# Performance work log

Hardware: AMD Instinct MI355X
Metric: run time of the kernel (lower is better)

The kernel has to match this reference:

```python
import jax, jax.numpy as jnp
import numpy as np

NEG_SLOPE = 0.2  # PyG GATConv default negative_slope


def _gat_layer(x, src, dst, W, a_src, a_dst, b, heads, ch, concat, num_nodes):
    # x: [Nt, Fin]; W: [Fin, heads*ch]; a_src/a_dst: [heads, ch]
    xw = (x @ W).reshape(num_nodes, heads, ch)            # [Nt, H, C]
    alpha_s = jnp.sum(xw * a_src, axis=-1)                # [Nt, H]
    alpha_d = jnp.sum(xw * a_dst, axis=-1)                # [Nt, H]
    e = jax.nn.leaky_relu(alpha_s[src] + alpha_d[dst], NEG_SLOPE)  # [E, H]
    # segment softmax over destination nodes (every node has a self-loop)
    m = jax.lax.stop_gradient(jax.ops.segment_max(e, dst, num_segments=num_nodes))
    ex = jnp.exp(e - m[dst])
    denom = jax.ops.segment_sum(ex, dst, num_segments=num_nodes)
    alpha = ex / (denom[dst] + 1e-16)                     # [E, H]
    out = jax.ops.segment_sum(alpha[:, :, None] * xw[src], dst, num_segments=num_nodes)  # [Nt, H, C]
    out = out.reshape(num_nodes, heads * ch) if concat else out.mean(axis=1)
    return out + b


def setup_inputs() -> dict:
    key = jax.random.key(0)
    ks = jax.random.split(key, 12)
    B, N, IN, HID, H, OUT, E = 2, 10000, 256, 256, 2, 256, 160000
    x = jax.random.normal(ks[0], (B, N, IN), dtype=jnp.float32)
    edge_index = jax.random.randint(ks[1], (2, E), 0, N, dtype=jnp.int32)
    s_in = 1.0 / np.sqrt(IN)
    s_h = 1.0 / np.sqrt(HID)
    s_hh = 1.0 / np.sqrt(HID * H)
    W1 = jax.random.normal(ks[2], (IN, H * HID), dtype=jnp.float32) * s_in
    att_src1 = jax.random.normal(ks[3], (H, HID), dtype=jnp.float32) * s_h
    att_dst1 = jax.random.normal(ks[4], (H, HID), dtype=jnp.float32) * s_h
    b1 = jax.random.normal(ks[5], (H * HID,), dtype=jnp.float32) * 0.01
    W2 = jax.random.normal(ks[6], (H * HID, OUT), dtype=jnp.float32) * s_hh
    att_src2 = jax.random.normal(ks[7], (1, OUT), dtype=jnp.float32) * s_h
    att_dst2 = jax.random.normal(ks[8], (1, OUT), dtype=jnp.float32) * s_h
    b2 = jax.random.normal(ks[9], (OUT,), dtype=jnp.float32) * 0.01
    return {"x": x, "edge_index": edge_index, "W1": W1, "att_src1": att_src1,
            "att_dst1": att_dst1, "b1": b1, "W2": W2, "att_src2": att_src2,
            "att_dst2": att_dst2, "b2": b2}


def reference(x, edge_index, W1, att_src1, att_dst1, b1, W2, att_src2, att_dst2, b2):
    B, N, C = x.shape
    H, HID = att_src1.shape
    OUT = W2.shape[1]
    Nt = B * N
    xf = x.reshape(Nt, C)
    # batch edge index with per-graph node offsets (shared edges across batch)
    offs = (jnp.arange(B, dtype=edge_index.dtype) * N)       # [B]
    ei = (edge_index[:, None, :] + offs[None, :, None]).reshape(2, -1)  # [2, B*E]
    # add self loops (PyG GATConv default)
    loops = jnp.arange(Nt, dtype=edge_index.dtype)
    src = jnp.concatenate([ei[0], loops])
    dst = jnp.concatenate([ei[1], loops])
    h = _gat_layer(xf, src, dst, W1, att_src1, att_dst1, b1, H, HID, True, Nt)
    h = jax.nn.gelu(h, approximate=False)  # torch F.gelu default = exact erf
    out = _gat_layer(h, src, dst, W2, att_src2, att_dst2, b2, 1, OUT, False, Nt)
    return out.reshape(B, N, OUT)
```

## Files before the change

### kernel.cpp

```cpp
#include <hip/hip_runtime.h>
#include <math.h>

constexpr int B_   = 2;
constexpr int N_   = 10000;
constexpr int IN_  = 256;
constexpr int HID_ = 256;
constexpr int H1_  = 2;
constexpr int OUT_ = 256;
constexpr int E_   = 160000;
constexpr int NT_  = B_ * N_;
constexpr float SLOPE = 0.2f;
constexpr int DMAX = 128;

typedef unsigned short u16;
typedef __attribute__((ext_vector_type(8))) short short8;
typedef __attribute__((ext_vector_type(4))) float f32x4;

__device__ __forceinline__ u16 f2bf(float f) {
    unsigned int u = __float_as_uint(f);
    u += 0x7fffu + ((u >> 16) & 1u);
    return (u16)(u >> 16);
}
__device__ __forceinline__ void bf8(uint4 r, float4& lo, float4& hi) {
    lo = make_float4(__uint_as_float((r.x & 0xffffu) << 16),
                     __uint_as_float(r.x & 0xffff0000u),
                     __uint_as_float((r.y & 0xffffu) << 16),
                     __uint_as_float(r.y & 0xffff0000u));
    hi = make_float4(__uint_as_float((r.z & 0xffffu) << 16),
                     __uint_as_float(r.z & 0xffff0000u),
                     __uint_as_float((r.w & 0xffffu) << 16),
                     __uint_as_float(r.w & 0xffff0000u));
}
__device__ __forceinline__ void fma4(float4& a, float s, float4 v) {
    a.x = fmaf(s, v.x, a.x); a.y = fmaf(s, v.y, a.y);
    a.z = fmaf(s, v.z, a.z); a.w = fmaf(s, v.w, a.w);
}
__device__ __forceinline__ float lrelu(float e) { return (e < 0.f) ? SLOPE * e : e; }

__device__ __forceinline__ void g2l16(const void* g, void* l) {
    __builtin_amdgcn_global_load_lds(
        (const __attribute__((address_space(1))) unsigned int*)g,
        (__attribute__((address_space(3))) unsigned int*)l, 16, 0, 0);
}

__global__ __launch_bounds__(256) void k_wprep(
    const float* __restrict__ W1,
    const float* __restrict__ aS1, const float* __restrict__ aD1,
    const float* __restrict__ W2,
    const float* __restrict__ aS2, const float* __restrict__ aD2,
    float* __restrict__ w1s, float* __restrict__ w1d,
    float* __restrict__ w2s, float* __restrict__ w2d,
    u16* __restrict__ W1t, u16* __restrict__ W2t,
    uint4* __restrict__ zbase) {
    __shared__ float tld[32][33];
    const int blk = blockIdx.x;
    if (blk < 16) {
        for (int i = blk * 256 + threadIdx.x; i < 12500; i += 16 * 256)
            zbase[i] = make_uint4(0, 0, 0, 0);
    } else if (blk < 528) {
        int wv = (blk - 16) * 4 + (threadIdx.x >> 6);
        int lane = threadIdx.x & 63;
        int c = lane * 4;
        float4 wr, av;
        if (wv < 1024) {
            int h = (wv >> 8) & 1;
            int k = wv & 255;
            const float* a = (wv < 512) ? aS1 : aD1;
            wr = *(const float4*)(W1 + (size_t)k * 512 + h * 256 + c);
            av = *(const float4*)(a + h * 256 + c);
        } else {
            int k = (wv - 1024) & 511;
            const float* a = (wv < 1536) ? aS2 : aD2;
            wr = *(const float4*)(W2 + (size_t)k * 256 + c);
            av = *(const float4*)(a + c);
        }
        float s = wr.x * av.x + wr.y * av.y + wr.z * av.z + wr.w * av.w;
        #pragma unroll
        for (int off = 32; off; off >>= 1) s += __shfl_down(s, off);
        if (lane == 0) {
            if (wv < 512)       w1s[wv] = s;
            else if (wv < 1024) w1d[wv - 512] = s;
            else if (wv < 1536) w2s[wv - 1024] = s;
            else                w2d[wv - 1536] = s;
        }
    } else {
        const int b = blk - 528;
        const int z = b >> 7;
        const int bb = b & 127;
        const float* S = z ? W2 : W1;
        u16* D = z ? W2t : W1t;
        const int R = z ? 512 : 256;
        const int C = z ? 256 : 512;
        const int xt = C >> 5;
        const int bx = bb % xt, by = bb / xt;
        const int tx = threadIdx.x & 31, ty = threadIdx.x >> 5;
        int xx = bx * 32 + tx;
        int y0 = by * 32 + ty;
        #pragma unroll
        for (int i = 0; i < 32; i += 8)
            tld[ty + i][tx] = S[(size_t)(y0 + i) * C + xx];
        __syncthreads();
        int xo = by * 32 + tx;
        int yo = bx * 32 + ty;
        #pragma unroll
        for (int i = 0; i < 32; i += 8)
            D[(size_t)(yo + i) * R + xo] = f2bf(tld[tx][ty + i]);
    }
}

__global__ __launch_bounds__(256) void k_pre(
    const float* __restrict__ x, u16* __restrict__ Xb,
    const float* __restrict__ w1s, const float* __restrict__ w1d,
    float* __restrict__ as1, float* __restrict__ ad1,
    const int* __restrict__ ei, int* __restrict__ cnt, int* __restrict__ bucket) {
    const int NB = NT_ / 4;
    if ((int)blockIdx.x < NB) {
        const int w = threadIdx.x >> 6, lane = threadIdx.x & 63;
        const int nt = blockIdx.x * 4 + w;
        const int c = lane * 4;
        float4 v = *(const float4*)(x + (size_t)nt * 256 + c);
        ((uint2*)(Xb + (size_t)nt * 256))[lane] =
            make_uint2((unsigned)f2bf(v.x) | ((unsigned)f2bf(v.y) << 16),
                       (unsigned)f2bf(v.z) | ((unsigned)f2bf(v.w) << 16));
        float4 s0v = *(const float4*)(w1s + c);
        float4 s1v = *(const float4*)(w1s + 256 + c);
        float4 d0v = *(const float4*)(w1d + c);
        float4 d1v = *(const float4*)(w1d + 256 + c);
        float s0 = v.x*s0v.x + v.y*s0v.y + v.z*s0v.z + v.w*s0v.w;
        float s1 = v.x*s1v.x + v.y*s1v.y + v.z*s1v.z + v.w*s1v.w;
        float d0 = v.x*d0v.x + v.y*d0v.y + v.z*d0v.z + v.w*d0v.w;
        float d1 = v.x*d1v.x + v.y*d1v.y + v.z*d1v.z + v.w*d1v.w;
        #pragma unroll
        for (int off = 32; off; off >>= 1) {
            s0 += __shfl_down(s0, off); s1 += __shfl_down(s1, off);
            d0 += __shfl_down(d0, off); d1 += __shfl_down(d1, off);
        }
        if (lane == 0) {
            as1[nt * 2] = s0; as1[nt * 2 + 1] = s1;
            ad1[nt * 2] = d0; ad1[nt * 2 + 1] = d1;
        }
    } else {
        int e = (blockIdx.x - NB) * 256 + threadIdx.x;
        if (e < E_) {
            int s = ei[e], d = ei[E_ + e];
            int p = atomicAdd(&cnt[d], 1);
            if (p < DMAX - 1) bucket[d * DMAX + p] = s;
        }
    }
}

__global__ __launch_bounds__(256) void k_agg1x(
    const u16* __restrict__ Xb,
    const float* __restrict__ as_, const float* __restrict__ ad_,
    const int* __restrict__ cnt, const int* __restrict__ bucket,
    u16* __restrict__ Y) {
    __shared__ int   stl[4][DMAX];
    __shared__ float exw[4][2 * DMAX];
    const int w    = threadIdx.x >> 6;
    const int lane = threadIdx.x & 63;
    const int half = lane >> 5;
    const int l32  = lane & 31;
    const int nt   = blockIdx.x * 4 + w;
    if (nt >= NT_) return;
    const int nl   = nt % N_;
    const int boff = nt - nl;
    const int r0   = nl * DMAX;
    int deg = cnt[nl]; deg = (deg < DMAX - 1) ? deg : (DMAX - 1);
    const float adv0 = ad_[nt * 2], adv1 = ad_[nt * 2 + 1];
    const float adv = half ? adv1 : adv0;

    for (int i = lane; i <= deg; i += 64)
        stl[w][i] = (i < deg) ? (bucket[r0 + i] + boff) : nt;

    float den = 0.f;
    for (int i = l32; i <= deg; i += 32) {
        int st = stl[w][i];
        float ex = __expf(lrelu(as_[st * 2 + half] + adv));
        exw[w][2 * i + half] = ex;
        den += ex;
    }
    #pragma unroll
    for (int off = 16; off; off >>= 1) den += __shfl_xor(den, off);
    const float inv = 1.f / (den + 1e-16f);
    const float invO = __shfl_xor(inv, 32);

    const int slot = half;
    const int nin = deg + 1;
    const u16* fb = Xb + l32 * 8;
    float4 A0l = {0,0,0,0}, A0h = {0,0,0,0}, A1l = {0,0,0,0}, A1h = {0,0,0,0};
    float4 B0l = {0,0,0,0}, B0h = {0,0,0,0}, B1l = {0,0,0,0}, B1h = {0,0,0,0};
    int j = 0;
    for (; j + 8 <= nin; j += 8) {
        int sA = stl[w][j + slot],     sB = stl[w][j + 2 + slot];
        int sC = stl[w][j + 4 + slot], sD = stl[w][j + 6 + slot];
        float2 wA = *(const float2*)&exw[w][2 * (j + slot)];
        float2 wB = *(const float2*)&exw[w][2 * (j + 2 + slot)];
        float2 wC = *(const float2*)&exw[w][2 * (j + 4 + slot)];
        float2 wD = *(const float2*)&exw[w][2 * (j + 6 + slot)];
        uint4 vA = *(const uint4*)(fb + (size_t)sA * 256);
        uint4 vB = *(const uint4*)(fb + (size_t)sB * 256);
        uint4 vC = *(const uint4*)(fb + (size_t)sC * 256);
        uint4 vD = *(const uint4*)(fb + (size_t)sD * 256);
        float4 lo, hi;
        bf8(vA, lo, hi); fma4(A0l, wA.x, lo); fma4(A0h, wA.x, hi);
                         fma4(A1l, wA.y, lo); fma4(A1h, wA.y, hi);
        bf8(vB, lo, hi); fma4(B0l, wB.x, lo); fma4(B0h, wB.x, hi);
                         fma4(B1l, wB.y, lo); fma4(B1h, wB.y, hi);
        bf8(vC, lo, hi); fma4(A0l, wC.x, lo); fma4(A0h, wC.x, hi);
                         fma4(A1l, wC.y, lo); fma4(A1h, wC.y, hi);
        bf8(vD, lo, hi); fma4(B0l, wD.x, lo); fma4(B0h, wD.x, hi);
                         fma4(B1l, wD.y, lo); fma4(B1h, wD.y, hi);
    }
    for (int jj = j + slot; jj < nin; jj += 2) {
        int s0 = stl[w][jj];
        float2 w01 = *(const float2*)&exw[w][2 * jj];
        uint4 v0 = *(const uint4*)(fb + (size_t)s0 * 256);
        float4 lo, hi;
        bf8(v0, lo, hi); fma4(A0l, w01.x, lo); fma4(A0h, w01.x, hi);
                         fma4(A1l, w01.y, lo); fma4(A1h, w01.y, hi);
    }
    A0l.x += B0l.x; A0l.y += B0l.y; A0l.z += B0l.z; A0l.w += B0l.w;
    A0h.x += B0h.x; A0h.y += B0h.y; A0h.z += B0h.z; A0h.w += B0h.w;
    A1l.x += B1l.x; A1l.y += B1l.y; A1l.z += B1l.z; A1l.w += B1l.w;
    A1h.x += B1h.x; A1h.y += B1h.y; A1h.z += B1h.z; A1h.w += B1h.w;
    A0l.x += __shfl_xor(A0l.x, 32); A0l.y += __shfl_xor(A0l.y, 32);
    A0l.z += __shfl_xor(A0l.z, 32); A0l.w += __shfl_xor(A0l.w, 32);
    A0h.x += __shfl_xor(A0h.x, 32); A0h.y += __shfl_xor(A0h.y, 32);
    A0h.z += __shfl_xor(A0h.z, 32); A0h.w += __shfl_xor(A0h.w, 32);
    A1l.x += __shfl_xor(A1l.x, 32); A1l.y += __shfl_xor(A1l.y, 32);
    A1l.z += __shfl_xor(A1l.z, 32); A1l.w += __shfl_xor(A1l.w, 32);
    A1h.x += __shfl_xor(A1h.x, 32); A1h.y += __shfl_xor(A1h.y, 32);
    A1h.z += __shfl_xor(A1h.z, 32); A1h.w += __shfl_xor(A1h.w, 32);

    if (slot == 0) {
        float f0[8] = { A0l.x*inv,  A0l.y*inv,  A0l.z*inv,  A0l.w*inv,
                        A0h.x*inv,  A0h.y*inv,  A0h.z*inv,  A0h.w*inv };
        float f1[8] = { A1l.x*invO, A1l.y*invO, A1l.z*invO, A1l.w*invO,
                        A1h.x*invO, A1h.y*invO, A1h.z*invO, A1h.w*invO };
        size_t ob = (size_t)nt * 512 + l32 * 8;
        *(uint4*)(Y + ob) =
            make_uint4((unsigned)f2bf(f0[0]) | ((unsigned)f2bf(f0[1]) << 16),
                       (unsigned)f2bf(f0[2]) | ((unsigned)f2bf(f0[3]) << 16),
                       (unsigned)f2bf(f0[4]) | ((unsigned)f2bf(f0[5]) << 16),
                       (unsigned)f2bf(f0[6]) | ((unsigned)f2bf(f0[7]) << 16));
        *(uint4*)(Y + ob + 256) =
            make_uint4((unsigned)f2bf(f1[0]) | ((unsigned)f2bf(f1[1]) << 16),
                       (unsigned)f2bf(f1[2]) | ((unsigned)f2bf(f1[3]) << 16),
                       (unsigned)f2bf(f1[4]) | ((unsigned)f2bf(f1[5]) << 16),
                       (unsigned)f2bf(f1[6]) | ((unsigned)f2bf(f1[7]) << 16));
    }
}

__global__ __launch_bounds__(256, 3) void gemm_g(
    const u16* __restrict__ Yf, const u16* __restrict__ W1t,
    u16* __restrict__ Hb,
    const float* __restrict__ b1,
    const float* __restrict__ w2s, const float* __restrict__ w2d,
    float* __restrict__ as2, float* __restrict__ ad2, int M) {
    __shared__ u16 sA[64 * 256];
    __shared__ u16 sBd[2][64 * 64];
    const int tid = threadIdx.x, wave = tid >> 6, lane = tid & 63;
    const int bm = blockIdx.x, h = blockIdx.y;
    const int wm = wave & 1, wn = wave >> 1;
    const int l15 = lane & 15, quad = lane >> 4;

    {
        const int rl = lane >> 5;
        const int u  = lane & 31;
        #pragma unroll
        for (int i = 0; i < 8; i++) {
            int rloc = wave * 16 + i * 2 + rl;
            int rg = bm * 64 + rloc; rg = (rg < M) ? rg : (M - 1);
            int us = (u & ~7) | ((u & 7) ^ (rloc & 7));
            g2l16(Yf + (size_t)rg * 512 + h * 256 + us * 8,
                  &sA[(wave * 16 + i * 2) * 256]);
        }
    }

    const int brl = lane >> 3;
    const int bu  = lane & 7;
    auto stageB = [&](int bn, int kb, int b) {
        #pragma unroll
        for (int i = 0; i < 2; i++) {
            int R0 = wave * 16 + i * 8;
            int r = R0 + brl;
            int us = bu ^ (r & 7);
            g2l16(W1t + (size_t)(h * 256 + bn * 64 + r) * 256 + kb * 64 + us * 8,
                  &sBd[b][R0 * 64]);
        }
    };

    const int rA0 = wm * 32 + l15, rA1 = rA0 + 16;
    const int rB0 = wn * 32 + l15, rB1 = rB0 + 16;

    f32x4 acc[2][2];
    #pragma unroll
    for (int i = 0; i < 2; i++)
        #pragma unroll
        for (int j = 0; j < 2; j++)
            acc[i][j] = (f32x4){0.f, 0.f, 0.f, 0.f};

    stageB(0, 0, 0);
    __syncthreads();
    int buf = 0;
    for (int bn = 0; bn < 4; bn++) {
        #pragma unroll
        for (int kb = 0; kb < 4; kb++) {
            int nbn = (kb == 3) ? bn + 1 : bn;
            int nkb = (kb == 3) ? 0 : kb + 1;
            if (nbn < 4) stageB(nbn, nkb, buf ^ 1);
            #pragma unroll
            for (int ks = 0; ks < 2; ks++) {
                int ua = kb * 8 + ks * 4 + quad;
                short8 a0 = *(const short8*)(&sA[rA0 * 256 + ((ua & ~7) | ((ua & 7) ^ (rA0 & 7))) * 8]);
                short8 a1 = *(const short8*)(&sA[rA1 * 256 + ((ua & ~7) | ((ua & 7) ^ (rA1 & 7))) * 8]);
                int ub = ks * 4 + quad;
                short8 b0  = *(const short8*)(&sBd[buf][rB0 * 64 + (ub ^ (rB0 & 7)) * 8]);
                short8 b1v = *(const short8*)(&sBd[buf][rB1 * 64 + (ub ^ (rB1 & 7)) * 8]);
                acc[0][0] = __builtin_amdgcn_mfma_f32_16x16x32_bf16(a0, b0,  acc[0][0], 0, 0, 0);
                acc[0][1] = __builtin_amdgcn_mfma_f32_16x16x32_bf16(a0, b1v, acc[0][1], 0, 0, 0);
                acc[1][0] = __builtin_amdgcn_mfma_f32_16x16x32_bf16(a1, b0,  acc[1][0], 0, 0, 0);
                acc[1][1] = __builtin_amdgcn_mfma_f32_16x16x32_bf16(a1, b1v, acc[1][1], 0, 0, 0);
            }
            if (kb == 3) {
                const int colL = bn * 64 + wn * 32;
                float Bv[2], Sv[2], Dv[2];
                #pragma unroll
                for (int j = 0; j < 2; j++) {
                    int cg = h * 256 + colL + j * 16 + l15;
                    Bv[j] = b1[cg]; Sv[j] = w2s[cg]; Dv[j] = w2d[cg];
                }
                #pragma unroll
                for (int i = 0; i < 2; i++) {
                    #pragma unroll
                    for (int r = 0; r < 4; r++) {
                        int row = bm * 64 + wm * 32 + i * 16 + quad * 4 + r;
                        float o[2], ps = 0.f, pd = 0.f;
                        #pragma unroll
                        for (int j = 0; j < 2; j++) {
                            float v = acc[i][j][r] + Bv[j];
                            v = 0.5f * v * (1.f + erff(v * 0.70710678118654752f));
                            o[j] = v;
                            ps = fmaf(v, Sv[j], ps);
                            pd = fmaf(v, Dv[j], pd);
                        }
                        #pragma unroll
                        for (int off = 1; off < 16; off <<= 1) {
                            ps += __shfl_xor(ps, off);
                            pd += __shfl_xor(pd, off);
                        }
                        if (row < M) {
                            if (l15 == 0) { atomicAdd(&as2[row], ps); atomicAdd(&ad2[row], pd); }
                            #pragma unroll
                            for (int j = 0; j < 2; j++)
                                Hb[(size_t)row * 512 + h * 256 + colL + j * 16 + l15] = f2bf(o[j]);
                        }
                    }
                }
                #pragma unroll
                for (int i = 0; i < 2; i++)
                    #pragma unroll
                    for (int j = 0; j < 2; j++)
                        acc[i][j] = (f32x4){0.f, 0.f, 0.f, 0.f};
            }
            __syncthreads();
            buf ^= 1;
        }
    }
}

__global__ __launch_bounds__(256, 3) void gemm_p(
    const u16* __restrict__ A, const u16* __restrict__ Bt,
    u16* __restrict__ C16, int M) {
    __shared__ u16 sA[32 * 512];
    __shared__ u16 sBd[2][64 * 64];
    const int tid = threadIdx.x, wave = tid >> 6, lane = tid & 63;
    const int bm = blockIdx.x;
    const int wm = wave & 1, wn = wave >> 1;
    const int l15 = lane & 15, quad = lane >> 4;

    {
        const int u = lane;
        #pragma unroll
        for (int i = 0; i < 8; i++) {
            int rloc = wave * 8 + i;
            int rg = bm * 32 + rloc; rg = (rg < M) ? rg : (M - 1);
            int us = (u & ~7) | ((u & 7) ^ (rloc & 7));
            g2l16(A + (size_t)rg * 512 + us * 8, &sA[rloc * 512]);
        }
    }

    const int brl = lane >> 3;
    const int bu  = lane & 7;
    auto stageB = [&](int bn, int kb, int b) {
        #pragma unroll
        for (int i = 0; i < 2; i++) {
            int R0 = wave * 16 + i * 8;
            int r = R0 + brl;
            int us = bu ^ (r & 7);
            g2l16(Bt + (size_t)(bn * 64 + r) * 512 + kb * 64 + us * 8,
                  &sBd[b][R0 * 64]);
        }
    };

    const int rA0 = wm * 16 + l15;
    const int rB0 = wn * 32 + l15, rB1 = rB0 + 16;

    f32x4 acc[2];
    acc[0] = (f32x4){0.f, 0.f, 0.f, 0.f};
    acc[1] = (f32x4){0.f, 0.f, 0.f, 0.f};

    stageB(0, 0, 0);
    __syncthreads();
    int buf = 0;
    for (int bn = 0; bn < 4; bn++) {
        #pragma unroll
        for (int kb = 0; kb < 8; kb++) {
            int nbn = (kb == 7) ? bn + 1 : bn;
            int nkb = (kb == 7) ? 0 : kb + 1;
            if (nbn < 4) stageB(nbn, nkb, buf ^ 1);
            #pragma unroll
            for (int ks = 0; ks < 2; ks++) {
                int ua = kb * 8 + ks * 4 + quad;
                short8 a0 = *(const short8*)(&sA[rA0 * 512 + ((ua & ~7) | ((ua & 7) ^ (rA0 & 7))) * 8]);
                int ub = ks * 4 + quad;
                short8 b0  = *(const short8*)(&sBd[buf][rB0 * 64 + (ub ^ (rB0 & 7)) * 8]);
                short8 b1v = *(const short8*)(&sBd[buf][rB1 * 64 + (ub ^ (rB1 & 7)) * 8]);
                acc[0] = __builtin_amdgcn_mfma_f32_16x16x32_bf16(a0, b0,  acc[0], 0, 0, 0);
                acc[1] = __builtin_amdgcn_mfma_f32_16x16x32_bf16(a0, b1v, acc[1], 0, 0, 0);
            }
            if (kb == 7) {
                #pragma unroll
                for (int r = 0; r < 4; r++) {
                    int row = bm * 32 + wm * 16 + quad * 4 + r;
                    if (row < M) {
                        #pragma unroll
                        for (int j = 0; j < 2; j++) {
                            int col = bn * 64 + wn * 32 + j * 16 + l15;
                            C16[(size_t)row * 256 + col] = f2bf(acc[j][r]);
                        }
                    }
                }
                acc[0] = (f32x4){0.f, 0.f, 0.f, 0.f};
                acc[1] = (f32x4){0.f, 0.f, 0.f, 0.f};
            }
            __syncthreads();
            buf ^= 1;
        }
    }
}

__global__ __launch_bounds__(256) void k_agg_h1(
    const u16* __restrict__ feat,
    const float* __restrict__ as_, const float* __restrict__ ad_,
    const int* __restrict__ cnt, const int* __restrict__ bucket,
    const float* __restrict__ bias,
    float* __restrict__ out) {
    __shared__ int   stl[4][DMAX];
    __shared__ float exw[4][DMAX];
    const int w    = threadIdx.x >> 6;
    const int lane = threadIdx.x & 63;
    const int slot = lane >> 5;
    const int l32  = lane & 31;
    const int nt   = blockIdx.x * 4 + w;
    if (nt >= NT_) return;
    const int nl   = nt % N_;
    const int boff = nt - nl;
    const int r0   = nl * DMAX;
    int deg = cnt[nl]; deg = (deg < DMAX - 1) ? deg : (DMAX - 1);
    const float adv = ad_[nt];

    for (int i = lane; i <= deg; i += 64)
        stl[w][i] = (i < deg) ? (bucket[r0 + i] + boff) : nt;

    float den = 0.f;
    for (int i = lane; i <= deg; i += 64) {
        int st = stl[w][i];
        float ex = __expf(lrelu(as_[st] + adv));
        exw[w][i] = ex;
        den += ex;
    }
    #pragma unroll
    for (int off = 32; off; off >>= 1) den += __shfl_xor(den, off);
    const float inv = 1.f / (den + 1e-16f);

    const int nin = deg + 1;
    const u16* fb = feat + l32 * 8;
    float4 aA0 = {0,0,0,0}, aB0 = {0,0,0,0}, aA1 = {0,0,0,0}, aB1 = {0,0,0,0};
    int j = 0;
    for (; j + 8 <= nin; j += 8) {
        int sA = stl[w][j + slot],     sB = stl[w][j + 2 + slot];
        int sC = stl[w][j + 4 + slot], sD = stl[w][j + 6 + slot];
        float wA = exw[w][j + slot],     wB = exw[w][j + 2 + slot];
        float wC = exw[w][j + 4 + slot], wD = exw[w][j + 6 + slot];
        uint4 vA = *(const uint4*)(fb + (size_t)sA * 256);
        uint4 vB = *(const uint4*)(fb + (size_t)sB * 256);
        uint4 vC = *(const uint4*)(fb + (size_t)sC * 256);
        uint4 vD = *(const uint4*)(fb + (size_t)sD * 256);
        float4 lo, hi;
        bf8(vA, lo, hi); fma4(aA0, wA, lo); fma4(aB0, wA, hi);
        bf8(vB, lo, hi); fma4(aA1, wB, lo); fma4(aB1, wB, hi);
        bf8(vC, lo, hi); fma4(aA0, wC, lo); fma4(aB0, wC, hi);
        bf8(vD, lo, hi); fma4(aA1, wD, lo); fma4(aB1, wD, hi);
    }
    for (; j + 4 <= nin; j += 4) {
        int sA = stl[w][j + slot], sB = stl[w][j + 2 + slot];
        float wA = exw[w][j + slot], wB = exw[w][j + 2 + slot];
        uint4 vA = *(const uint4*)(fb + (size_t)sA * 256);
        uint4 vB = *(const uint4*)(fb + (size_t)sB * 256);
        float4 lo, hi;
        bf8(vA, lo, hi); fma4(aA0, wA, lo); fma4(aB0, wA, hi);
        bf8(vB, lo, hi); fma4(aA1, wB, lo); fma4(aB1, wB, hi);
    }
    for (int jj = j + slot; jj < nin; jj += 2) {
        int s0 = stl[w][jj];
        float w0 = exw[w][jj];
        uint4 v0 = *(const uint4*)(fb + (size_t)s0 * 256);
        float4 lo, hi;
        bf8(v0, lo, hi); fma4(aA0, w0, lo); fma4(aB0, w0, hi);
    }
    aA0.x += aA1.x; aA0.y += aA1.y; aA0.z += aA1.z; aA0.w += aA1.w;
    aB0.x += aB1.x; aB0.y += aB1.y; aB0.z += aB1.z; aB0.w += aB1.w;
    aA0.x += __shfl_xor(aA0.x, 32); aA0.y += __shfl_xor(aA0.y, 32);
    aA0.z += __shfl_xor(aA0.z, 32); aA0.w += __shfl_xor(aA0.w, 32);
    aB0.x += __shfl_xor(aB0.x, 32); aB0.y += __shfl_xor(aB0.y, 32);
    aB0.z += __shfl_xor(aB0.z, 32); aB0.w += __shfl_xor(aB0.w, 32);

    if (slot == 0) {
        int c = l32 * 8;
        float4 b0 = *(const float4*)(bias + c);
        float4 b1 = *(const float4*)(bias + c + 4);
        float* ob = out + (size_t)nt * 256 + c;
        *(float4*)(ob)     = make_float4(aA0.x * inv + b0.x, aA0.y * inv + b0.y,
                                         aA0.z * inv + b0.z, aA0.w * inv + b0.w);
        *(float4*)(ob + 4) = make_float4(aB0.x * inv + b1.x, aB0.y * inv + b1.y,
                                         aB0.z * inv + b1.z, aB0.w * inv + b1.w);
    }
}

extern "C" void kernel_launch(void* const* d_in, const int* in_sizes, int n_in,
                              void* d_out, int out_size, void* d_ws, size_t ws_size,
                              hipStream_t stream) {
    const float* x    = (const float*)d_in[0];
    const int*   ei   = (const int*)  d_in[1];
    const float* W1   = (const float*)d_in[2];
    const float* aS1  = (const float*)d_in[3];
    const float* aD1  = (const float*)d_in[4];
    const float* b1   = (const float*)d_in[5];
    const float* W2   = (const float*)d_in[6];
    const float* aS2  = (const float*)d_in[7];
    const float* aD2  = (const float*)d_in[8];
    const float* b2   = (const float*)d_in[9];
    float* out = (float*)d_out;

    u16* Xb   = (u16*)d_ws;
    u16* Y    = Xb + (size_t)NT_ * 256;
    u16* Hb   = Y  + (size_t)NT_ * 512;
    u16* hw16 = Hb + (size_t)NT_ * 512;
    float* as1 = (float*)(hw16 + (size_t)NT_ * 256);
    float* ad1 = as1 + NT_ * H1_;
    float* as2 = ad1 + NT_ * H1_;
    float* ad2 = as2 + NT_;
    int* cnt   = (int*)(ad2 + NT_);
    int* bucket= cnt + N_;
    u16* W1t   = (u16*)(bucket + N_ * DMAX);
    u16* W2t   = W1t + 512 * 256;
    float* w1s = (float*)(W2t + 256 * 512);
    float* w1d = w1s + 512;
    float* w2s = w1d + 512;
    float* w2d = w2s + 512;

    k_wprep<<<784, 256, 0, stream>>>(W1, aS1, aD1, W2, aS2, aD2,
                                     w1s, w1d, w2s, w2d, W1t, W2t, (uint4*)as2);

    k_pre<<<NT_ / 4 + (E_ + 255) / 256, 256, 0, stream>>>(
        x, Xb, w1s, w1d, as1, ad1, ei, cnt, bucket);

    k_agg1x<<<(NT_ + 3) / 4, 256, 0, stream>>>(Xb, as1, ad1, cnt, bucket, Y);
    gemm_g<<<dim3((NT_ + 63) / 64, 2), 256, 0, stream>>>(
        Y, W1t, Hb, b1, w2s, w2d, as2, ad2, NT_);

    gemm_p<<<dim3((NT_ + 31) / 32), 256, 0, stream>>>(Hb, W2t, hw16, NT_);
    k_agg_h1<<<(NT_ + 3) / 4, 256, 0, stream>>>(hw16, as2, ad2, cnt, bucket, b2, out);
}
```

Measured before the change: 192.1 us.

## Split aggregation kernels into four column slices with 8-row-parallel gather per wave

Both edge-aggregation kernels now launch four blocks per group of nodes, and each block handles one 64-column slice of the 256-wide features. Within a wave, 8 lanes cover a slice and 8 neighbour rows are gathered in parallel, then reduced with xor-shuffles. The aim is more parallelism and memory-level concurrency per node, since average degree is about 9, and less per-thread serial looping. In exchange, the softmax weights and neighbour list are recomputed four times per node, the unrolled multi-accumulator loops are dropped, and the cross-lane reduction is deeper.

Measured after the change: 240.3 us. +25.1%, slower.

```diff
diff --git a/kernel.cpp b/kernel.cpp
--- a/kernel.cpp
+++ b/kernel.cpp
@@ -149,25 +149,26 @@
     }
 }
 
-__global__ __launch_bounds__(256) void k_agg1x(
+__global__ __launch_bounds__(256) void k_agg1s(
     const u16* __restrict__ Xb,
     const float* __restrict__ as_, const float* __restrict__ ad_,
     const int* __restrict__ cnt, const int* __restrict__ bucket,
     u16* __restrict__ Y) {
     __shared__ int   stl[4][DMAX];
     __shared__ float exw[4][2 * DMAX];
-    const int w    = threadIdx.x >> 6;
-    const int lane = threadIdx.x & 63;
-    const int half = lane >> 5;
-    const int l32  = lane & 31;
-    const int nt   = blockIdx.x * 4 + w;
+    const int slice = blockIdx.x & 3;
+    const int grp   = blockIdx.x >> 2;
+    const int w     = threadIdx.x >> 6;
+    const int lane  = threadIdx.x & 63;
+    const int half  = lane >> 5;
+    const int l32   = lane & 31;
+    const int nt    = grp * 4 + w;
     if (nt >= NT_) return;
     const int nl   = nt % N_;
     const int boff = nt - nl;
     const int r0   = nl * DMAX;
     int deg = cnt[nl]; deg = (deg < DMAX - 1) ? deg : (DMAX - 1);
-    const float adv0 = ad_[nt * 2], adv1 = ad_[nt * 2 + 1];
-    const float adv = half ? adv1 : adv0;
+    const float adv = half ? ad_[nt * 2 + 1] : ad_[nt * 2];
 
     for (int i = lane; i <= deg; i += 64)
         stl[w][i] = (i < deg) ? (bucket[r0 + i] + boff) : nt;
@@ -181,63 +182,45 @@
     }
     #pragma unroll
     for (int off = 16; off; off >>= 1) den += __shfl_xor(den, off);
-    const float inv = 1.f / (den + 1e-16f);
-    const float invO = __shfl_xor(inv, 32);
-
-    const int slot = half;
-    const int nin = deg + 1;
-    const u16* fb = Xb + l32 * 8;
-    float4 A0l = {0,0,0,0}, A0h = {0,0,0,0}, A1l = {0,0,0,0}, A1h = {0,0,0,0};
-    float4 B0l = {0,0,0,0}, B0h = {0,0,0,0}, B1l = {0,0,0,0}, B1h = {0,0,0,0};
-    int j = 0;
-    for (; j + 8 <= nin; j += 8) {
-        int sA = stl[w][j + slot],     sB = stl[w][j + 2 + slot];
-        int sC = stl[w][j + 4 + slot], sD = stl[w][j + 6 + slot];
-        float2 wA = *(const float2*)&exw[w][2 * (j + slot)];
-        float2 wB = *(const float2*)&exw[w][2 * (j + 2 + slot)];
-        float2 wC = *(const float2*)&exw[w][2 * (j + 4 + slot)];
-        float2 wD = *(const float2*)&exw[w][2 * (j + 6 + slot)];
-        uint4 vA = *(const uint4*)(fb + (size_t)sA * 256);
-        uint4 vB = *(const uint4*)(fb + (size_t)sB * 256);
-        uint4 vC = *(const uint4*)(fb + (size_t)sC * 256);
-        uint4 vD = *(const uint4*)(fb + (size_t)sD * 256);
-        float4 lo, hi;
-        bf8(vA, lo, hi); fma4(A0l, wA.x, lo); fma4(A0h, wA.x, hi);
-                         fma4(A1l, wA.y, lo); fma4(A1h, wA.y, hi);
-        bf8(vB, lo, hi); fma4(B0l, wB.x, lo); fma4(B0h, wB.x, hi);
-                         fma4(B1l, wB.y, lo); fma4(B1h, wB.y, hi);
-        bf8(vC, lo, hi); fma4(A0l, wC.x, lo); fma4(A0h, wC.x, hi);
-                         fma4(A1l, wC.y, lo); fma4(A1h, wC.y, hi);
-        bf8(vD, lo, hi); fma4(B0l, wD.x, lo); fma4(B0h, wD.x, hi);
-                         fma4(B1l, wD.y, lo); fma4(B1h, wD.y, hi);
-    }
-    for (int jj = j + slot; jj < nin; jj += 2) {
-        int s0 = stl[w][jj];
-        float2 w01 = *(const float2*)&exw[w][2 * jj];
-        uint4 v0 = *(const uint4*)(fb + (size_t)s0 * 256);
-        float4 lo, hi;
-        bf8(v0, lo, hi); fma4(A0l, w01.x, lo); fma4(A0h, w01.x, hi);
-                         fma4(A1l, w01.y, lo); fma4(A1h, w01.y, hi);
-    }
-    A0l.x += B0l.x; A0l.y += B0l.y; A0l.z += B0l.z; A0l.w += B0l.w;
-    A0h.x += B0h.x; A0h.y += B0h.y; A0h.z += B0h.z; A0h.w += B0h.w;
-    A1l.x += B1l.x; A1l.y += B1l.y; A1l.z += B1l.z; A1l.w += B1l.w;
-    A1h.x += B1h.x; A1h.y += B1h.y; A1h.z += B1h.z; A1h.w += B1h.w;
-    A0l.x += __shfl_xor(A0l.x, 32); A0l.y += __shfl_xor(A0l.y, 32);
-    A0l.z += __shfl_xor(A0l.z, 32); A0l.w += __shfl_xor(A0l.w, 32);
-    A0h.x += __shfl_xor(A0h.x, 32); A0h.y += __shfl_xor(A0h.y, 32);
-    A0h.z += __shfl_xor(A0h.z, 32); A0h.w += __shfl_xor(A0h.w, 32);
-    A1l.x += __shfl_xor(A1l.x, 32); A1l.y += __shfl_xor(A1l.y, 32);
-    A1l.z += __shfl_xor(A1l.z, 32); A1l.w += __shfl_xor(A1l.w, 32);
-    A1h.x += __shfl_xor(A1h.x, 32); A1h.y += __shfl_xor(A1h.y, 32);
-    A1h.z += __shfl_xor(A1h.z, 32); A1h.w += __shfl_xor(A1h.w, 32);
-
-    if (slot == 0) {
-        float f0[8] = { A0l.x*inv,  A0l.y*inv,  A0l.z*inv,  A0l.w*inv,
-                        A0h.x*inv,  A0h.y*inv,  A0h.z*inv,  A0h.w*inv };
-        float f1[8] = { A1l.x*invO, A1l.y*invO, A1l.z*invO, A1l.w*invO,
-                        A1h.x*invO, A1h.y*invO, A1h.z*invO, A1h.w*invO };
-        size_t ob = (size_t)nt * 512 + l32 * 8;
+    const float inv  = 1.f / (den + 1e-16f);
+    const float inv0 = __shfl(inv, 0);
+    const float inv1 = __shfl(inv, 32);
+
+    const int rs = lane >> 3;
+    const int u  = lane & 7;
+    const u16* fb = Xb + slice * 64 + u * 8;
+    float4 a0l = {0,0,0,0}, a0h = {0,0,0,0};
+    float4 a1l = {0,0,0,0}, a1h = {0,0,0,0};
+    for (int j = 0; j <= deg; j += 8) {
+        int i = j + rs;
+        if (i <= deg) {
+            int st = stl[w][i];
+            float2 wp = *(const float2*)&exw[w][2 * i];
+            uint4 v = *(const uint4*)(fb + (size_t)st * 256);
+            float4 lo, hi;
+            bf8(v, lo, hi);
+            fma4(a0l, wp.x, lo); fma4(a0h, wp.x, hi);
+            fma4(a1l, wp.y, lo); fma4(a1h, wp.y, hi);
+        }
+    }
+    #pragma unroll
+    for (int off = 8; off < 64; off <<= 1) {
+        a0l.x += __shfl_xor(a0l.x, off); a0l.y += __shfl_xor(a0l.y, off);
+        a0l.z += __shfl_xor(a0l.z, off); a0l.w += __shfl_xor(a0l.w, off);
+        a0h.x += __shfl_xor(a0h.x, off); a0h.y += __shfl_xor(a0h.y, off);
+        a0h.z += __shfl_xor(a0h.z, off); a0h.w += __shfl_xor(a0h.w, off);
+        a1l.x += __shfl_xor(a1l.x, off); a1l.y += __shfl_xor(a1l.y, off);
+        a1l.z += __shfl_xor(a1l.z, off); a1l.w += __shfl_xor(a1l.w, off);
+        a1h.x += __shfl_xor(a1h.x, off); a1h.y += __shfl_xor(a1h.y, off);
+        a1h.z += __shfl_xor(a1h.z, off); a1h.w += __shfl_xor(a1h.w, off);
+    }
+
+    if (rs == 0) {
+        float f0[8] = { a0l.x*inv0, a0l.y*inv0, a0l.z*inv0, a0l.w*inv0,
+                        a0h.x*inv0, a0h.y*inv0, a0h.z*inv0, a0h.w*inv0 };
+        float f1[8] = { a1l.x*inv1, a1l.y*inv1, a1l.z*inv1, a1l.w*inv1,
+                        a1h.x*inv1, a1h.y*inv1, a1h.z*inv1, a1h.w*inv1 };
+        size_t ob = (size_t)nt * 512 + slice * 64 + u * 8;
         *(uint4*)(Y + ob) =
             make_uint4((unsigned)f2bf(f0[0]) | ((unsigned)f2bf(f0[1]) << 16),
                        (unsigned)f2bf(f0[2]) | ((unsigned)f2bf(f0[3]) << 16),
@@ -450,7 +433,7 @@
     }
 }
 
-__global__ __launch_bounds__(256) void k_agg_h1(
+__global__ __launch_bounds__(256) void k_agg2s(
     const u16* __restrict__ feat,
     const float* __restrict__ as_, const float* __restrict__ ad_,
     const int* __restrict__ cnt, const int* __restrict__ bucket,
@@ -458,11 +441,11 @@
     float* __restrict__ out) {
     __shared__ int   stl[4][DMAX];
     __shared__ float exw[4][DMAX];
-    const int w    = threadIdx.x >> 6;
-    const int lane = threadIdx.x & 63;
-    const int slot = lane >> 5;
-    const int l32  = lane & 31;
-    const int nt   = blockIdx.x * 4 + w;
+    const int slice = blockIdx.x & 3;
+    const int grp   = blockIdx.x >> 2;
+    const int w     = threadIdx.x >> 6;
+    const int lane  = threadIdx.x & 63;
+    const int nt    = grp * 4 + w;
     if (nt >= NT_) return;
     const int nl   = nt % N_;
     const int boff = nt - nl;
@@ -484,57 +467,38 @@
     for (int off = 32; off; off >>= 1) den += __shfl_xor(den, off);
     const float inv = 1.f / (den + 1e-16f);
 
-    const int nin = deg + 1;
-    const u16* fb = feat + l32 * 8;
-    float4 aA0 = {0,0,0,0}, aB0 = {0,0,0,0}, aA1 = {0,0,0,0}, aB1 = {0,0,0,0};
-    int j = 0;
-    for (; j + 8 <= nin; j += 8) {
-        int sA = stl[w][j + slot],     sB = stl[w][j + 2 + slot];
-        int sC = stl[w][j + 4 + slot], sD = stl[w][j + 6 + slot];
-        float wA = exw[w][j + slot],     wB = exw[w][j + 2 + slot];
-        float wC = exw[w][j + 4 + slot], wD = exw[w][j + 6 + slot];
-        uint4 vA = *(const uint4*)(fb + (size_t)sA * 256);
-        uint4 vB = *(const uint4*)(fb + (size_t)sB * 256);
-        uint4 vC = *(const uint4*)(fb + (size_t)sC * 256);
-        uint4 vD = *(const uint4*)(fb + (size_t)sD * 256);
-        float4 lo, hi;
-        bf8(vA, lo, hi); fma4(aA0, wA, lo); fma4(aB0, wA, hi);
-        bf8(vB, lo, hi); fma4(aA1, wB, lo); fma4(aB1, wB, hi);
-        bf8(vC, lo, hi); fma4(aA0, wC, lo); fma4(aB0, wC, hi);
-        bf8(vD, lo, hi); fma4(aA1, wD, lo); fma4(aB1, wD, hi);
-    }
-    for (; j + 4 <= nin; j += 4) {
-        int sA = stl[w][j + slot], sB = stl[w][j + 2 + slot];
-        float wA = exw[w][j + slot], wB = exw[w][j + 2 + slot];
-        uint4 vA = *(const uint4*)(fb + (size_t)sA * 256);
-        uint4 vB = *(const uint4*)(fb + (size_t)sB * 256);
-        float4 lo, hi;
-        bf8(vA, lo, hi); fma4(aA0, wA, lo); fma4(aB0, wA, hi);
-        bf8(vB, lo, hi); fma4(aA1, wB, lo); fma4(aB1, wB, hi);
-    }
-    for (int jj = j + slot; jj < nin; jj += 2) {
-        int s0 = stl[w][jj];
-        float w0 = exw[w][jj];
-        uint4 v0 = *(const uint4*)(fb + (size_t)s0 * 256);
-        float4 lo, hi;
-        bf8(v0, lo, hi); fma4(aA0, w0, lo); fma4(aB0, w0, hi);
-    }
-    aA0.x += aA1.x; aA0.y += aA1.y; aA0.z += aA1.z; aA0.w += aA1.w;
-    aB0.x += aB1.x; aB0.y += aB1.y; aB0.z += aB1.z; aB0.w += aB1.w;
-    aA0.x += __shfl_xor(aA0.x, 32); aA0.y += __shfl_xor(aA0.y, 32);
-    aA0.z += __shfl_xor(aA0.z, 32); aA0.w += __shfl_xor(aA0.w, 32);
-    aB0.x += __shfl_xor(aB0.x, 32); aB0.y += __shfl_xor(aB0.y, 32);
-    aB0.z += __shfl_xor(aB0.z, 32); aB0.w += __shfl_xor(aB0.w, 32);
-
-    if (slot == 0) {
-        int c = l32 * 8;
+    const int rs = lane >> 3;
+    const int u  = lane & 7;
+    const u16* fb = feat + slice * 64 + u * 8;
+    float4 al = {0,0,0,0}, ah = {0,0,0,0};
+    for (int j = 0; j <= deg; j += 8) {
+        int i = j + rs;
+        if (i <= deg) {
+            int st = stl[w][i];
+            float w0 = exw[w][i];
+            uint4 v = *(const uint4*)(fb + (size_t)st * 256);
+            float4 lo, hi;
+            bf8(v, lo, hi);
+            fma4(al, w0, lo); fma4(ah, w0, hi);
+        }
+    }
+    #pragma unroll
+    for (int off = 8; off < 64; off <<= 1) {
+        al.x += __shfl_xor(al.x, off); al.y += __shfl_xor(al.y, off);
+        al.z += __shfl_xor(al.z, off); al.w += __shfl_xor(al.w, off);
+        ah.x += __shfl_xor(ah.x, off); ah.y += __shfl_xor(ah.y, off);
+        ah.z += __shfl_xor(ah.z, off); ah.w += __shfl_xor(ah.w, off);
+    }
+
+    if (rs == 0) {
+        int c = slice * 64 + u * 8;
         float4 b0 = *(const float4*)(bias + c);
         float4 b1 = *(const float4*)(bias + c + 4);
         float* ob = out + (size_t)nt * 256 + c;
-        *(float4*)(ob)     = make_float4(aA0.x * inv + b0.x, aA0.y * inv + b0.y,
-                                         aA0.z * inv + b0.z, aA0.w * inv + b0.w);
-        *(float4*)(ob + 4) = make_float4(aB0.x * inv + b1.x, aB0.y * inv + b1.y,
-                                         aB0.z * inv + b1.z, aB0.w * inv + b1.w);
+        *(float4*)(ob)     = make_float4(al.x * inv + b0.x, al.y * inv + b0.y,
+                                         al.z * inv + b0.z, al.w * inv + b0.w);
+        *(float4*)(ob + 4) = make_float4(ah.x * inv + b1.x, ah.y * inv + b1.y,
+                                         ah.z * inv + b1.z, ah.w * inv + b1.w);
     }
 }
 
@@ -576,10 +540,11 @@
     k_pre<<<NT_ / 4 + (E_ + 255) / 256, 256, 0, stream>>>(
         x, Xb, w1s, w1d, as1, ad1, ei, cnt, bucket);
 
-    k_agg1x<<<(NT_ + 3) / 4, 256, 0, stream>>>(Xb, as1, ad1, cnt, bucket, Y);
+    k_agg1s<<<4 * ((NT_ + 3) / 4), 256, 0, stream>>>(Xb, as1, ad1, cnt, bucket, Y);
     gemm_g<<<dim3((NT_ + 63) / 64, 2), 256, 0, stream>>>(
         Y, W1t, Hb, b1, w2s, w2d, as2, ad2, NT_);
 
     gemm_p<<<dim3((NT_ + 31) / 32), 256, 0, stream>>>(Hb, W2t, hw16, NT_);
-    k_agg_h1<<<(NT_ + 3) / 4, 256, 0, stream>>>(hw16, as2, ad2, cnt, bucket, b2, out);
-}
+    k_agg2s<<<4 * ((NT_ + 3) / 4), 256, 0, stream>>>(
+        hw16, as2, ad2, cnt, bucket, b2, out);
+}
```
